# Performance work log

Hardware: AMD Instinct MI355X
Metric: run time of the kernel (lower is better)

## Reference

```python
import jax, jax.numpy as jnp
import numpy as np

CH = 128          # channels
R1 = 8            # ch_reduction1 -> theta/phi dim = 16
R2 = 2            # ch_reduction2 -> g dim = 64
D = 2             # downsampling (maxpool kernel/stride on w,h)


def _conv1x1x1(x, w, b):
    # x: (b, cin, n, w, h); w: (cout, cin); b: (cout,)
    return jnp.einsum('bcnwh,oc->bonwh', x, w) + b[None, :, None, None, None]


def _maxpool_wh(x):
    # 2x2 max pool (stride 2) over the last two dims; x: (b, c, n, w, h)
    b, c, n, w, h = x.shape
    return x.reshape(b, c, n, w // D, D, h // D, D).max(axis=(4, 6))


def setup_inputs() -> dict:
    key = jax.random.key(0)
    ks = jax.random.split(key, 9)
    c1, c2 = CH // R1, CH // R2
    s = lambda fan: 1.0 / np.sqrt(fan)
    return {
        'x': jax.random.normal(ks[0], (2, CH, 16, 32, 32), jnp.float32),
        'w_theta': jax.random.normal(ks[1], (c1, CH), jnp.float32) * s(CH),
        'b_theta': jnp.zeros((c1,), jnp.float32),
        'w_phi': jax.random.normal(ks[2], (c1, CH), jnp.float32) * s(CH),
        'b_phi': jnp.zeros((c1,), jnp.float32),
        'w_g': jax.random.normal(ks[3], (c2, CH), jnp.float32) * s(CH),
        'b_g': jnp.zeros((c2,), jnp.float32),
        'w_attn_g': jax.random.normal(ks[4], (CH, c2), jnp.float32) * s(c2),
        'b_attn_g': jnp.zeros((CH,), jnp.float32),
        'gamma': jnp.zeros((1,), jnp.float32),  # initial_gamma = 0
    }


def reference(x, w_theta, b_theta, w_phi, b_phi, w_g, b_g, w_attn_g, b_attn_g, gamma):
    bs, ch, n, w, h = x.shape
    N = n * w * h                       # query locations
    M = n * (w // D) * (h // D)         # pooled key/value locations

    # theta: (bs, N, c1)
    theta = jnp.tanh(_conv1x1x1(x, w_theta, b_theta))
    theta = theta.transpose(0, 2, 3, 4, 1).reshape(bs, N, -1)

    # phi: tanh proj -> maxpool over w,h -> (bs, M, c1)
    phi = _maxpool_wh(jnp.tanh(_conv1x1x1(x, w_phi, b_phi)))
    phi = phi.transpose(0, 2, 3, 4, 1).reshape(bs, M, -1)

    # dot-product kernel; softmax over dim=1 (QUERY axis), as in the torch code
    attn = jax.nn.softmax(jnp.einsum('bnc,bmc->bnm', theta, phi), axis=1)

    # g: proj -> maxpool -> (bs, M, c2)
    g = _maxpool_wh(_conv1x1x1(x, w_g, b_g))
    g = g.transpose(0, 2, 3, 4, 1).reshape(bs, M, -1)

    # attend and fold back to (bs, c2, n, w, h)
    attn_g = jnp.einsum('bnm,bmc->bnc', attn, g)
    attn_g = attn_g.reshape(bs, n, w, h, -1).transpose(0, 4, 1, 2, 3)
    attn_g = _conv1x1x1(attn_g, w_attn_g, b_attn_g)

    alpha = jax.nn.sigmoid(gamma)[0]
    out = (1.0 - alpha) * x + alpha * attn_g
    return (out, attn_g)
```

## Files before the change

### kernel.cpp

```cpp
#include <hip/hip_runtime.h>

typedef short bf16x8 __attribute__((ext_vector_type(8)));
typedef float f32x16 __attribute__((ext_vector_type(16)));

#define DI __device__ __forceinline__

constexpr int BS = 2, CH = 128;
constexpr int NQ = 16384, NM = 4096;
constexpr size_t NX = (size_t)BS * CH * NQ;

DI float bf2f(ushort u) { unsigned v = ((unsigned)u) << 16; return __builtin_bit_cast(float, v); }
DI ushort f2bf(float f) {
  unsigned u = __builtin_bit_cast(unsigned, f);
  u += 0x7FFFu + ((u >> 16) & 1u);
  return (ushort)(u >> 16);
}
DI float ldany(const void* p, size_t i, int f) {
  return f ? ((const float*)p)[i] : bf2f(((const ushort*)p)[i]);
}
DI f32x16 mfma_bf16(bf16x8 a, bf16x8 b, f32x16 c) {
  return __builtin_amdgcn_mfma_f32_32x32x16_bf16(a, b, c, 0, 0, 0);
}
DI float fexp2(float x) { return __builtin_amdgcn_exp2f(x); }

DI int sniff_local(const void* x) {
  const ushort* u = (const ushort*)x;
  int garbage = 0, zeros = 0;
  for (int i = 0; i < 256; ++i) {
    float v = bf2f(u[i]);
    if (!(fabsf(v) < 1e9f)) garbage++;
    if ((i & 1) == 0 && u[i] == 0) zeros++;
  }
  return (garbage >= 8 || zeros >= 100) ? 1 : 0;
}

__global__ __launch_bounds__(256) void k_prep(
    const void* __restrict__ x,
    const void* __restrict__ wT, const void* __restrict__ bT,
    const void* __restrict__ wP, const void* __restrict__ bP,
    const void* __restrict__ wG, const void* __restrict__ bG,
    const void* __restrict__ wAG, const void* __restrict__ bAG,
    int* __restrict__ flag,
    float* __restrict__ bAllf, uint4* __restrict__ wF, uint4* __restrict__ wBf)
{
  int t = threadIdx.x;
  __shared__ int fsh;
  if (t == 0) {
    int f = sniff_local(x);
    fsh = f;
    if (blockIdx.x == 0) flag[0] = f;
  }
  __syncthreads();
  int f = fsh;

  if (blockIdx.x == 0) {
    if (t < 16)  bAllf[t]       = ldany(bT, t, f);
    if (t < 16)  bAllf[16 + t]  = ldany(bP, t, f);
    if (t < 64)  bAllf[32 + t]  = ldany(bG, t, f);
    if (t < 128) bAllf[96 + t]  = ldany(bAG, t, f);
  } else if (blockIdx.x <= 4) {
    int idx = (blockIdx.x - 1) * 256 + t;
    int lane = idx & 63, ks = (idx >> 6) & 3, ot = idx >> 8;
    size_t src = (size_t)(ot * 32 + (lane & 31)) * 64 + ks * 16 + (lane >> 5) * 8;
    union { uint4 v4; ushort s[8]; } o;
    #pragma unroll
    for (int j = 0; j < 8; ++j) o.s[j] = f2bf(ldany(wAG, src + j, f));
    wF[idx] = o.v4;
  } else {
    int idx = (int)(blockIdx.x - 5) * 256 + t;
    int kb = idx / 192, rem = idx % 192;
    int ob = rem >> 6, lane = rem & 63;
    int r = ob * 32 + (lane & 31);
    int c = kb * 16 + (lane >> 5) * 8;
    const void* src; int row;
    if (r < 16)      { src = wT; row = r; }
    else if (r < 32) { src = wP; row = r - 16; }
    else             { src = wG; row = r - 32; }
    union { uint4 v4; ushort s[8]; } o;
    #pragma unroll
    for (int j = 0; j < 8; ++j) o.s[j] = f2bf(ldany(src, (size_t)row * 128 + c + j, f));
    wBf[(kb * 3 + ob) * 64 + lane] = o.v4;
  }
}

__global__ __launch_bounds__(256) void k_proj(
    const void* __restrict__ x, const int* __restrict__ flag,
    const uint4* __restrict__ wBf, const float* __restrict__ bAllf,
    ushort* __restrict__ theta, ushort* __restrict__ phi, ushort* __restrict__ gm)
{
  int b = blockIdx.y;
  int qt = blockIdx.x;
  int t = threadIdx.x;
  int w = t >> 6, l = t & 63, lr = l & 31, lh = l >> 5;
  int qhalf = w & 1, khalf = w >> 1;
  int f = flag[0];

  __shared__ float tile[64][33];

  size_t xbase = (size_t)b * CH * NQ + qt * 64 + qhalf * 32 + lr;

  f32x16 acc0, acc1, acc2;
  #pragma unroll
  for (int i = 0; i < 16; ++i) { acc0[i] = 0.f; acc1[i] = 0.f; acc2[i] = 0.f; }

  #pragma unroll
  for (int kk = 0; kk < 4; ++kk) {
    int kb = khalf * 4 + kk;
    union { uint4 v4; ushort s[8]; } a;
    int cb = kb * 16 + lh * 8;
    if (f) {
      const float* xf = (const float*)x;
      #pragma unroll
      for (int j = 0; j < 8; ++j) a.s[j] = f2bf(xf[xbase + (size_t)(cb + j) * NQ]);
    } else {
      const ushort* xu = (const ushort*)x;
      #pragma unroll
      for (int j = 0; j < 8; ++j) a.s[j] = xu[xbase + (size_t)(cb + j) * NQ];
    }
    bf16x8 aF = __builtin_bit_cast(bf16x8, a.v4);
    uint4 b0 = wBf[(kb * 3 + 0) * 64 + l];
    uint4 b1 = wBf[(kb * 3 + 1) * 64 + l];
    uint4 b2 = wBf[(kb * 3 + 2) * 64 + l];
    acc0 = mfma_bf16(aF, __builtin_bit_cast(bf16x8, b0), acc0);
    acc1 = mfma_bf16(aF, __builtin_bit_cast(bf16x8, b1), acc1);
    acc2 = mfma_bf16(aF, __builtin_bit_cast(bf16x8, b2), acc2);
  }

  constexpr float L2E = 1.4426950408889634f;

  #pragma unroll
  for (int ob = 0; ob < 3; ++ob) {
    f32x16 A = (ob == 0) ? acc0 : ((ob == 1) ? acc1 : acc2);
    __syncthreads();
    if (khalf == 1) {
      #pragma unroll
      for (int r = 0; r < 16; ++r) {
        int qq = (r & 3) + 8 * (r >> 2) + 4 * lh;
        tile[qhalf * 32 + qq][lr] = A[r];
      }
    }
    __syncthreads();
    if (khalf == 0) {
      #pragma unroll
      for (int r = 0; r < 16; ++r) {
        int qq = (r & 3) + 8 * (r >> 2) + 4 * lh;
        tile[qhalf * 32 + qq][lr] += A[r];
      }
    }
    __syncthreads();
    if (ob == 0) {
      if (t < 64) {
        union { uint4 v4[2]; ushort s[16]; } th;
        #pragma unroll
        for (int c = 0; c < 16; ++c)
          th.s[c] = f2bf(tanhf(tile[t][c] + bAllf[c]) * L2E);
        uint4* dst = (uint4*)(theta + ((size_t)b * NQ + qt * 64 + t) * 16);
        dst[0] = th.v4[0]; dst[1] = th.v4[1];
      } else if (t < 128) {
        int idx = t - 64;
        int m = idx >> 2, c4 = (idx & 3) * 4;
        int h2 = m * 2;
        union { uint2 v2; ushort s[4]; } ph;
        #pragma unroll
        for (int cc = 0; cc < 4; ++cc) {
          int c = 16 + c4 + cc;
          float z = fmaxf(fmaxf(tile[h2][c], tile[h2 + 1][c]),
                          fmaxf(tile[32 + h2][c], tile[32 + h2 + 1][c]));
          ph.s[cc] = f2bf(tanhf(z + bAllf[c]));
        }
        *(uint2*)(phi + ((size_t)b * NM + qt * 16 + m) * 16 + c4) = ph.v2;
      }
    } else {
      if (t < 128) {
        int cb = (ob - 1) * 32;
        int m = t >> 3, c4 = (t & 7) * 4;
        int h2 = m * 2;
        union { uint2 v2; ushort s[4]; } gv;
        #pragma unroll
        for (int cc = 0; cc < 4; ++cc) {
          int c = c4 + cc;
          float z = fmaxf(fmaxf(tile[h2][c], tile[h2 + 1][c]),
                          fmaxf(tile[32 + h2][c], tile[32 + h2 + 1][c]));
          gv.s[cc] = f2bf(z + bAllf[32 + cb + c]);
        }
        *(uint2*)(gm + ((size_t)b * NM + qt * 16 + m) * 64 + cb + c4) = gv.v2;
      }
    }
  }
}

__global__ __launch_bounds__(1024, 2) void k_denom2(
    const ushort* __restrict__ theta, const ushort* __restrict__ phi,
    const ushort* __restrict__ gm, uint4* __restrict__ gsF)
{
  int b = blockIdx.y, mb = blockIdx.x;
  int t = threadIdx.x;
  int w = t >> 6, l = t & 63, lr = l & 31, lh = l >> 5;
  int mbase = mb * 32;

  __shared__ float part[16][33];
  __shared__ float dinv_sh[32];
  __shared__ float tile[32][65];

  bf16x8 pB = __builtin_bit_cast(bf16x8, *(const uint4*)(phi + ((size_t)b * NM + mbase + lr) * 16 + lh * 8));
  const ushort* thb = theta + ((size_t)b * NQ + w * 1024 + lr) * 16 + lh * 8;

  bf16x8 tA1 = __builtin_bit_cast(bf16x8, *(const uint4*)(thb + 512));
  f32x16 S;
  #pragma unroll
  for (int i = 0; i < 16; ++i) S[i] = 0.f;
  S = mfma_bf16(__builtin_bit_cast(bf16x8, *(const uint4*)thb), pB, S);

  float s = 0.f;
  for (int it = 0; it < 32; ++it) {
    bf16x8 tA2 = __builtin_bit_cast(bf16x8, *(const uint4*)(thb + (size_t)((it + 2) & 31) * 512));
    __builtin_amdgcn_sched_barrier(0);
    f32x16 Sn;
    #pragma unroll
    for (int i = 0; i < 16; ++i) Sn[i] = 0.f;
    Sn = mfma_bf16(tA1, pB, Sn);
    #pragma unroll
    for (int r = 0; r < 16; ++r) s += fexp2(S[r]);
    S = Sn; tA1 = tA2;
  }
  s += __shfl_xor(s, 32, 64);
  if (l < 32) part[w][lr] = s;
  __syncthreads();

  if (t < 32) {
    float d = 0.f;
    #pragma unroll
    for (int p = 0; p < 16; ++p) d += part[p][t];
    dinv_sh[t] = 1.f / d;
  }
  __syncthreads();

  if (t < 256) {
    int m_loc = t >> 3, c = (t & 7) * 8;
    union { uint4 v4; ushort s[8]; } v;
    v.v4 = *(const uint4*)(gm + ((size_t)b * NM + mbase + m_loc) * 64 + c);
    float dv = dinv_sh[m_loc];
    #pragma unroll
    for (int j = 0; j < 8; ++j) tile[m_loc][c + j] = bf2f(v.s[j]) * dv;
  }
  __syncthreads();

  if (t < 256) {
    int ms_loc = t >> 7, ct = (t >> 6) & 1, lane = t & 63;
    int col = ct * 32 + (lane & 31);
    int rbase = ms_loc * 16 + (lane >> 5) * 8;
    union { uint4 v4; ushort s[8]; } o;
    #pragma unroll
    for (int j = 0; j < 8; ++j) o.s[j] = f2bf(tile[rbase + j][col]);
    int ms = (mbase >> 4) + ms_loc;
    gsF[(((size_t)b * 256 + ms) * 2 + ct) * 64 + lane] = o.v4;
  }
}

__global__ __launch_bounds__(256, 3) void k_attn(
    const ushort* __restrict__ theta, const ushort* __restrict__ phi,
    const uint4* __restrict__ gsF, const uint4* __restrict__ wF,
    const float* __restrict__ bAllf, const void* __restrict__ x,
    const void* __restrict__ gamma, const int* __restrict__ flag,
    void* __restrict__ out_base)
{
  int b = blockIdx.y;
  int q0 = blockIdx.x * 64;
  int t = threadIdx.x;
  int mq = t >> 6, l = t & 63, lr = l & 31, lh = l >> 5;

  __shared__ float agPart[4][32][65];
  __shared__ __align__(16) ushort agF[32][80];

  bf16x8 tB0 = __builtin_bit_cast(bf16x8, *(const uint4*)(theta + ((size_t)b * NQ + q0 + lr) * 16 + lh * 8));
  bf16x8 tB1 = __builtin_bit_cast(bf16x8, *(const uint4*)(theta + ((size_t)b * NQ + q0 + 32 + lr) * 16 + lh * 8));

  const ushort* phb = phi + ((size_t)b * NM + lr) * 16 + lh * 8;
  const uint4* gF = gsF + (size_t)b * 32768;

  f32x16 a00, a01, a10, a11;
  #pragma unroll
  for (int i = 0; i < 16; ++i) { a00[i] = 0.f; a01[i] = 0.f; a10[i] = 0.f; a11[i] = 0.f; }
  f32x16 zero16;
  #pragma unroll
  for (int i = 0; i < 16; ++i) zero16[i] = 0.f;

  size_t gb0 = (size_t)(mq * 2) * 128;
  uint4 g00 = gF[gb0 + l];
  uint4 g01 = gF[gb0 + 64 + l];
  uint4 g10 = gF[gb0 + 128 + l];
  uint4 g11 = gF[gb0 + 192 + l];
  bf16x8 pA = __builtin_bit_cast(bf16x8, *(const uint4*)(phb + (size_t)(mq * 32) * 16));

  for (int it = 0; it < 32; ++it) {
    int it1 = (it + 1) & 31;
    size_t gb = (size_t)(mq * 2 + it1 * 8) * 128;
    uint4 n00 = gF[gb + l];
    uint4 n01 = gF[gb + 64 + l];
    uint4 n10 = gF[gb + 128 + l];
    uint4 n11 = gF[gb + 192 + l];
    bf16x8 pAn = __builtin_bit_cast(bf16x8, *(const uint4*)(phb + (size_t)(mq * 32 + it1 * 128) * 16));
    __builtin_amdgcn_sched_barrier(0);

    f32x16 Sa = mfma_bf16(pA, tB0, zero16);
    f32x16 Sb = mfma_bf16(pA, tB1, zero16);

    uint u0, u1, u2, u3, u4, u5, u6, u7;

    #pragma unroll
    for (int r = 0; r < 16; ++r) Sa[r] = fexp2(Sa[r]);
    asm("v_cvt_pk_bf16_f32 %0, %1, %2" : "=v"(u0) : "v"(Sa[0]),  "v"(Sa[1]));
    asm("v_cvt_pk_bf16_f32 %0, %1, %2" : "=v"(u1) : "v"(Sa[2]),  "v"(Sa[3]));
    asm("v_cvt_pk_bf16_f32 %0, %1, %2" : "=v"(u2) : "v"(Sa[4]),  "v"(Sa[5]));
    asm("v_cvt_pk_bf16_f32 %0, %1, %2" : "=v"(u3) : "v"(Sa[6]),  "v"(Sa[7]));
    asm("v_cvt_pk_bf16_f32 %0, %1, %2" : "=v"(u4) : "v"(Sa[8]),  "v"(Sa[9]));
    asm("v_cvt_pk_bf16_f32 %0, %1, %2" : "=v"(u5) : "v"(Sa[10]), "v"(Sa[11]));
    asm("v_cvt_pk_bf16_f32 %0, %1, %2" : "=v"(u6) : "v"(Sa[12]), "v"(Sa[13]));
    asm("v_cvt_pk_bf16_f32 %0, %1, %2" : "=v"(u7) : "v"(Sa[14]), "v"(Sa[15]));
    asm("v_permlane32_swap_b32 %0, %1" : "+v"(u0), "+v"(u2));
    asm("v_permlane32_swap_b32 %0, %1" : "+v"(u1), "+v"(u3));
    asm("v_permlane32_swap_b32 %0, %1" : "+v"(u4), "+v"(u6));
    asm("v_permlane32_swap_b32 %0, %1" : "+v"(u5), "+v"(u7));
    {
      uint4 fa0 = make_uint4(u0, u1, u2, u3);
      uint4 fa1 = make_uint4(u4, u5, u6, u7);
      a00 = mfma_bf16(__builtin_bit_cast(bf16x8, fa0), __builtin_bit_cast(bf16x8, g00), a00);
      a01 = mfma_bf16(__builtin_bit_cast(bf16x8, fa0), __builtin_bit_cast(bf16x8, g01), a01);
      a00 = mfma_bf16(__builtin_bit_cast(bf16x8, fa1), __builtin_bit_cast(bf16x8, g10), a00);
      a01 = mfma_bf16(__builtin_bit_cast(bf16x8, fa1), __builtin_bit_cast(bf16x8, g11), a01);
    }

    #pragma unroll
    for (int r = 0; r < 16; ++r) Sb[r] = fexp2(Sb[r]);
    asm("v_cvt_pk_bf16_f32 %0, %1, %2" : "=v"(u0) : "v"(Sb[0]),  "v"(Sb[1]));
    asm("v_cvt_pk_bf16_f32 %0, %1, %2" : "=v"(u1) : "v"(Sb[2]),  "v"(Sb[3]));
    asm("v_cvt_pk_bf16_f32 %0, %1, %2" : "=v"(u2) : "v"(Sb[4]),  "v"(Sb[5]));
    asm("v_cvt_pk_bf16_f32 %0, %1, %2" : "=v"(u3) : "v"(Sb[6]),  "v"(Sb[7]));
    asm("v_cvt_pk_bf16_f32 %0, %1, %2" : "=v"(u4) : "v"(Sb[8]),  "v"(Sb[9]));
    asm("v_cvt_pk_bf16_f32 %0, %1, %2" : "=v"(u5) : "v"(Sb[10]), "v"(Sb[11]));
    asm("v_cvt_pk_bf16_f32 %0, %1, %2" : "=v"(u6) : "v"(Sb[12]), "v"(Sb[13]));
    asm("v_cvt_pk_bf16_f32 %0, %1, %2" : "=v"(u7) : "v"(Sb[14]), "v"(Sb[15]));
    asm("v_permlane32_swap_b32 %0, %1" : "+v"(u0), "+v"(u2));
    asm("v_permlane32_swap_b32 %0, %1" : "+v"(u1), "+v"(u3));
    asm("v_permlane32_swap_b32 %0, %1" : "+v"(u4), "+v"(u6));
    asm("v_permlane32_swap_b32 %0, %1" : "+v"(u5), "+v"(u7));
    {
      uint4 fb0 = make_uint4(u0, u1, u2, u3);
      uint4 fb1 = make_uint4(u4, u5, u6, u7);
      a10 = mfma_bf16(__builtin_bit_cast(bf16x8, fb0), __builtin_bit_cast(bf16x8, g00), a10);
      a11 = mfma_bf16(__builtin_bit_cast(bf16x8, fb0), __builtin_bit_cast(bf16x8, g01), a11);
      a10 = mfma_bf16(__builtin_bit_cast(bf16x8, fb1), __builtin_bit_cast(bf16x8, g10), a10);
      a11 = mfma_bf16(__builtin_bit_cast(bf16x8, fb1), __builtin_bit_cast(bf16x8, g11), a11);
    }

    pA = pAn;
    g00 = n00; g01 = n01; g10 = n10; g11 = n11;
  }

  int mode = flag[0];
  float ga = ldany(gamma, 0, mode);
  float alpha = 1.f / (1.f + __expf(-ga));

  #pragma unroll
  for (int h = 0; h < 2; ++h) {
    __syncthreads();
    {
      f32x16 ac0 = (h == 0) ? a00 : a10;
      f32x16 ac1 = (h == 0) ? a01 : a11;
      #pragma unroll
      for (int r = 0; r < 16; ++r) {
        int qq = (r & 3) + 8 * (r >> 2) + 4 * lh;
        agPart[mq][qq][lr]      = ac0[r];
        agPart[mq][qq][32 + lr] = ac1[r];
      }
    }
    __syncthreads();
    {
      #pragma unroll
      for (int jj = 0; jj < 8; ++jj) {
        int c = mq * 16 + lh * 8 + jj;
        float vsum = agPart[0][lr][c] + agPart[1][lr][c] + agPart[2][lr][c] + agPart[3][lr][c];
        agF[lr][c] = f2bf(vsum);
      }
    }
    __syncthreads();
    {
      f32x16 oacc;
      #pragma unroll
      for (int i = 0; i < 16; ++i) oacc[i] = 0.f;
      #pragma unroll
      for (int ks = 0; ks < 4; ++ks) {
        bf16x8 aw = __builtin_bit_cast(bf16x8, wF[(mq * 4 + ks) * 64 + l]);
        bf16x8 bg = __builtin_bit_cast(bf16x8, *(const uint4*)&agF[lr][ks * 16 + lh * 8]);
        oacc = mfma_bf16(aw, bg, oacc);
      }
      if (mode) {
        float* o0 = (float*)out_base;
        float* o1 = o0 + NX;
        const float* xf = (const float*)x;
        #pragma unroll
        for (int r = 0; r < 16; ++r) {
          int o = mq * 32 + (r & 3) + 8 * (r >> 2) + 4 * lh;
          size_t oi = ((size_t)b * CH + o) * NQ + q0 + h * 32 + lr;
          float ag = oacc[r] + bAllf[96 + o];
          o0[oi] = (1.f - alpha) * xf[oi] + alpha * ag;
          o1[oi] = ag;
        }
      } else {
        ushort* o0 = (ushort*)out_base;
        ushort* o1 = o0 + NX;
        const ushort* xu = (const ushort*)x;
        #pragma unroll
        for (int r = 0; r < 16; ++r) {
          int o = mq * 32 + (r & 3) + 8 * (r >> 2) + 4 * lh;
          size_t oi = ((size_t)b * CH + o) * NQ + q0 + h * 32 + lr;
          float ag = oacc[r] + bAllf[96 + o];
          o0[oi] = f2bf((1.f - alpha) * bf2f(xu[oi]) + alpha * ag);
          o1[oi] = f2bf(ag);
        }
      }
    }
  }
}

extern "C" void kernel_launch(void* const* d_in, const int* in_sizes, int n_in,
                              void* d_out, int out_size, void* d_ws, size_t ws_size,
                              hipStream_t stream) {
  const void* x    = d_in[0];
  const void* wT   = d_in[1];
  const void* bT   = d_in[2];
  const void* wP   = d_in[3];
  const void* bP   = d_in[4];
  const void* wG   = d_in[5];
  const void* bG   = d_in[6];
  const void* wAG  = d_in[7];
  const void* bAG  = d_in[8];
  const void* gmm  = d_in[9];

  char* ws = (char*)d_ws;
  ushort* theta  = (ushort*)(ws + 0);
  ushort* phi    = (ushort*)(ws + 1048576);
  ushort* gm     = (ushort*)(ws + 1310720);
  uint4*  gsF    = (uint4*) (ws + 3407872);
  uint4*  wF     = (uint4*) (ws + 4456448);
  uint4*  wBf    = (uint4*) (ws + 4472832);
  float*  bAllf  = (float*) (ws + 4497408);
  int*    flag   = (int*)   (ws + 4498432);

  k_prep<<<dim3(11), dim3(256), 0, stream>>>(x, wT, bT, wP, bP, wG, bG, wAG, bAG, flag, bAllf, wF, wBf);
  k_proj<<<dim3(256, 2), dim3(256), 0, stream>>>(x, flag, wBf, bAllf, theta, phi, gm);
  k_denom2<<<dim3(128, 2), dim3(1024), 0, stream>>>(theta, phi, gm, gsF);
  k_attn<<<dim3(256, 2), dim3(256), 0, stream>>>(theta, phi, gsF, wF, bAllf, x, gmm, flag, d_out);
}
```

Baseline: 73.21 us.

## Fold prep kernel into projection and attention kernels; remap attn blocks per XCD

Removes the separate k_prep launch. Each block of k_proj and k_attn now sniffs the input dtype in parallel and converts the weights and biases it needs into LDS. This eliminates one kernel launch and its serial dependency, and moves weight reads from global to LDS. In exchange every block repeats the weight conversion work. k_attn also switches to a 1D grid whose block index maps onto XCDs, so that each XCD handles contiguous query tiles of one batch for better L2 locality.

```diff
diff --git a/kernel.cpp b/kernel.cpp
--- a/kernel.cpp
+++ b/kernel.cpp
@@ -23,51 +23,40 @@
 }
 DI float fexp2(float x) { return __builtin_amdgcn_exp2f(x); }
 
-DI int sniff_local(const void* x) {
+DI int sniff_block(const void* x, int t, int* cnt_sh) {
   const ushort* u = (const ushort*)x;
-  int garbage = 0, zeros = 0;
-  for (int i = 0; i < 256; ++i) {
-    float v = bf2f(u[i]);
-    if (!(fabsf(v) < 1e9f)) garbage++;
-    if ((i & 1) == 0 && u[i] == 0) zeros++;
-  }
-  return (garbage >= 8 || zeros >= 100) ? 1 : 0;
-}
-
-__global__ __launch_bounds__(256) void k_prep(
+  if (t == 0) { cnt_sh[0] = 0; cnt_sh[1] = 0; }
+  __syncthreads();
+  if (t < 256) {
+    float v = bf2f(u[t]);
+    if (!(fabsf(v) < 1e9f)) atomicAdd(&cnt_sh[0], 1);
+    if (((t & 1) == 0) && (u[t] == 0)) atomicAdd(&cnt_sh[1], 1);
+  }
+  __syncthreads();
+  return (cnt_sh[0] >= 8 || cnt_sh[1] >= 100) ? 1 : 0;
+}
+
+__global__ __launch_bounds__(256) void k_proj(
     const void* __restrict__ x,
     const void* __restrict__ wT, const void* __restrict__ bT,
     const void* __restrict__ wP, const void* __restrict__ bP,
     const void* __restrict__ wG, const void* __restrict__ bG,
-    const void* __restrict__ wAG, const void* __restrict__ bAG,
-    int* __restrict__ flag,
-    float* __restrict__ bAllf, uint4* __restrict__ wF, uint4* __restrict__ wBf)
+    ushort* __restrict__ theta, ushort* __restrict__ phi, ushort* __restrict__ gm)
 {
+  int b = blockIdx.y;
+  int qt = blockIdx.x;
   int t = threadIdx.x;
-  __shared__ int fsh;
-  if (t == 0) {
-    int f = sniff_local(x);
-    fsh = f;
-    if (blockIdx.x == 0) flag[0] = f;
-  }
-  __syncthreads();
-  int f = fsh;
-
-  if (blockIdx.x == 0) {
-    if (t < 16)  bAllf[t]       = ldany(bT, t, f);
-    if (t < 16)  bAllf[16 + t]  = ldany(bP, t, f);
-    if (t < 64)  bAllf[32 + t]  = ldany(bG, t, f);
-    if (t < 128) bAllf[96 + t]  = ldany(bAG, t, f);
-  } else if (blockIdx.x <= 4) {
-    int idx = (blockIdx.x - 1) * 256 + t;
-    int lane = idx & 63, ks = (idx >> 6) & 3, ot = idx >> 8;
-    size_t src = (size_t)(ot * 32 + (lane & 31)) * 64 + ks * 16 + (lane >> 5) * 8;
-    union { uint4 v4; ushort s[8]; } o;
-    #pragma unroll
-    for (int j = 0; j < 8; ++j) o.s[j] = f2bf(ldany(wAG, src + j, f));
-    wF[idx] = o.v4;
-  } else {
-    int idx = (int)(blockIdx.x - 5) * 256 + t;
+  int w = t >> 6, l = t & 63, lr = l & 31, lh = l >> 5;
+  int qhalf = w & 1, khalf = w >> 1;
+
+  __shared__ int cnt_sh[2];
+  __shared__ __align__(16) uint4 wBf_sh[24][64];
+  __shared__ float bias_sh[96];
+  __shared__ float tile[64][33];
+
+  int f = sniff_block(x, t, cnt_sh);
+
+  for (int idx = t; idx < 1536; idx += 256) {
     int kb = idx / 192, rem = idx % 192;
     int ob = rem >> 6, lane = rem & 63;
     int r = ob * 32 + (lane & 31);
@@ -79,23 +68,12 @@
     union { uint4 v4; ushort s[8]; } o;
     #pragma unroll
     for (int j = 0; j < 8; ++j) o.s[j] = f2bf(ldany(src, (size_t)row * 128 + c + j, f));
-    wBf[(kb * 3 + ob) * 64 + lane] = o.v4;
-  }
-}
-
-__global__ __launch_bounds__(256) void k_proj(
-    const void* __restrict__ x, const int* __restrict__ flag,
-    const uint4* __restrict__ wBf, const float* __restrict__ bAllf,
-    ushort* __restrict__ theta, ushort* __restrict__ phi, ushort* __restrict__ gm)
-{
-  int b = blockIdx.y;
-  int qt = blockIdx.x;
-  int t = threadIdx.x;
-  int w = t >> 6, l = t & 63, lr = l & 31, lh = l >> 5;
-  int qhalf = w & 1, khalf = w >> 1;
-  int f = flag[0];
-
-  __shared__ float tile[64][33];
+    wBf_sh[kb * 3 + ob][lane] = o.v4;
+  }
+  if (t < 16)       bias_sh[t] = ldany(bT, t, f);
+  else if (t < 32)  bias_sh[t] = ldany(bP, t - 16, f);
+  else if (t < 96)  bias_sh[t] = ldany(bG, t - 32, f);
+  __syncthreads();
 
   size_t xbase = (size_t)b * CH * NQ + qt * 64 + qhalf * 32 + lr;
 
@@ -118,9 +96,9 @@
       for (int j = 0; j < 8; ++j) a.s[j] = xu[xbase + (size_t)(cb + j) * NQ];
     }
     bf16x8 aF = __builtin_bit_cast(bf16x8, a.v4);
-    uint4 b0 = wBf[(kb * 3 + 0) * 64 + l];
-    uint4 b1 = wBf[(kb * 3 + 1) * 64 + l];
-    uint4 b2 = wBf[(kb * 3 + 2) * 64 + l];
+    uint4 b0 = wBf_sh[kb * 3 + 0][l];
+    uint4 b1 = wBf_sh[kb * 3 + 1][l];
+    uint4 b2 = wBf_sh[kb * 3 + 2][l];
     acc0 = mfma_bf16(aF, __builtin_bit_cast(bf16x8, b0), acc0);
     acc1 = mfma_bf16(aF, __builtin_bit_cast(bf16x8, b1), acc1);
     acc2 = mfma_bf16(aF, __builtin_bit_cast(bf16x8, b2), acc2);
@@ -153,7 +131,7 @@
         union { uint4 v4[2]; ushort s[16]; } th;
         #pragma unroll
         for (int c = 0; c < 16; ++c)
-          th.s[c] = f2bf(tanhf(tile[t][c] + bAllf[c]) * L2E);
+          th.s[c] = f2bf(tanhf(tile[t][c] + bias_sh[c]) * L2E);
         uint4* dst = (uint4*)(theta + ((size_t)b * NQ + qt * 64 + t) * 16);
         dst[0] = th.v4[0]; dst[1] = th.v4[1];
       } else if (t < 128) {
@@ -166,7 +144,7 @@
           int c = 16 + c4 + cc;
           float z = fmaxf(fmaxf(tile[h2][c], tile[h2 + 1][c]),
                           fmaxf(tile[32 + h2][c], tile[32 + h2 + 1][c]));
-          ph.s[cc] = f2bf(tanhf(z + bAllf[c]));
+          ph.s[cc] = f2bf(tanhf(z + bias_sh[c]));
         }
         *(uint2*)(phi + ((size_t)b * NM + qt * 16 + m) * 16 + c4) = ph.v2;
       }
@@ -181,7 +159,7 @@
           int c = c4 + cc;
           float z = fmaxf(fmaxf(tile[h2][c], tile[h2 + 1][c]),
                           fmaxf(tile[32 + h2][c], tile[32 + h2 + 1][c]));
-          gv.s[cc] = f2bf(z + bAllf[32 + cb + c]);
+          gv.s[cc] = f2bf(z + bias_sh[32 + cb + c]);
         }
         *(uint2*)(gm + ((size_t)b * NM + qt * 16 + m) * 64 + cb + c4) = gv.v2;
       }
@@ -259,18 +237,35 @@
 
 __global__ __launch_bounds__(256, 3) void k_attn(
     const ushort* __restrict__ theta, const ushort* __restrict__ phi,
-    const uint4* __restrict__ gsF, const uint4* __restrict__ wF,
-    const float* __restrict__ bAllf, const void* __restrict__ x,
-    const void* __restrict__ gamma, const int* __restrict__ flag,
-    void* __restrict__ out_base)
+    const uint4* __restrict__ gsF, const void* __restrict__ wAG,
+    const void* __restrict__ bAG, const void* __restrict__ x,
+    const void* __restrict__ gamma, void* __restrict__ out_base)
 {
-  int b = blockIdx.y;
-  int q0 = blockIdx.x * 64;
+  int idx = blockIdx.x;
+  int xcd = idx & 7, slot = idx >> 3;
+  int b = xcd >> 2;
+  int q0 = ((xcd & 3) * 64 + slot) * 64;
   int t = threadIdx.x;
   int mq = t >> 6, l = t & 63, lr = l & 31, lh = l >> 5;
 
+  __shared__ int cnt_sh[2];
+  __shared__ __align__(16) uint4 wF_lds[16][64];
+  __shared__ float bag_sh[128];
   __shared__ float agPart[4][32][65];
   __shared__ __align__(16) ushort agF[32][80];
+
+  int f = sniff_block(x, t, cnt_sh);
+
+  for (int i = t; i < 1024; i += 256) {
+    int lane = i & 63, ks = (i >> 6) & 3, ot = i >> 8;
+    size_t src = (size_t)(ot * 32 + (lane & 31)) * 64 + ks * 16 + (lane >> 5) * 8;
+    union { uint4 v4; ushort s[8]; } o;
+    #pragma unroll
+    for (int j = 0; j < 8; ++j) o.s[j] = f2bf(ldany(wAG, src + j, f));
+    wF_lds[ot * 4 + ks][lane] = o.v4;
+  }
+  if (t < 128) bag_sh[t] = ldany(bAG, t, f);
+  __syncthreads();
 
   bf16x8 tB0 = __builtin_bit_cast(bf16x8, *(const uint4*)(theta + ((size_t)b * NQ + q0 + lr) * 16 + lh * 8));
   bf16x8 tB1 = __builtin_bit_cast(bf16x8, *(const uint4*)(theta + ((size_t)b * NQ + q0 + 32 + lr) * 16 + lh * 8));
@@ -357,8 +352,7 @@
     g00 = n00; g01 = n01; g10 = n10; g11 = n11;
   }
 
-  int mode = flag[0];
-  float ga = ldany(gamma, 0, mode);
+  float ga = ldany(gamma, 0, f);
   float alpha = 1.f / (1.f + __expf(-ga));
 
   #pragma unroll
@@ -390,11 +384,11 @@
       for (int i = 0; i < 16; ++i) oacc[i] = 0.f;
       #pragma unroll
       for (int ks = 0; ks < 4; ++ks) {
-        bf16x8 aw = __builtin_bit_cast(bf16x8, wF[(mq * 4 + ks) * 64 + l]);
+        bf16x8 aw = __builtin_bit_cast(bf16x8, wF_lds[mq * 4 + ks][l]);
         bf16x8 bg = __builtin_bit_cast(bf16x8, *(const uint4*)&agF[lr][ks * 16 + lh * 8]);
         oacc = mfma_bf16(aw, bg, oacc);
       }
-      if (mode) {
+      if (f) {
         float* o0 = (float*)out_base;
         float* o1 = o0 + NX;
         const float* xf = (const float*)x;
@@ -402,7 +396,7 @@
         for (int r = 0; r < 16; ++r) {
           int o = mq * 32 + (r & 3) + 8 * (r >> 2) + 4 * lh;
           size_t oi = ((size_t)b * CH + o) * NQ + q0 + h * 32 + lr;
-          float ag = oacc[r] + bAllf[96 + o];
+          float ag = oacc[r] + bag_sh[o];
           o0[oi] = (1.f - alpha) * xf[oi] + alpha * ag;
           o1[oi] = ag;
         }
@@ -414,7 +408,7 @@
         for (int r = 0; r < 16; ++r) {
           int o = mq * 32 + (r & 3) + 8 * (r >> 2) + 4 * lh;
           size_t oi = ((size_t)b * CH + o) * NQ + q0 + h * 32 + lr;
-          float ag = oacc[r] + bAllf[96 + o];
+          float ag = oacc[r] + bag_sh[o];
           o0[oi] = f2bf((1.f - alpha) * bf2f(xu[oi]) + alpha * ag);
           o1[oi] = f2bf(ag);
         }
@@ -442,13 +436,8 @@
   ushort* phi    = (ushort*)(ws + 1048576);
   ushort* gm     = (ushort*)(ws + 1310720);
   uint4*  gsF    = (uint4*) (ws + 3407872);
-  uint4*  wF     = (uint4*) (ws + 4456448);
-  uint4*  wBf    = (uint4*) (ws + 4472832);
-  float*  bAllf  = (float*) (ws + 4497408);
-  int*    flag   = (int*)   (ws + 4498432);
-
-  k_prep<<<dim3(11), dim3(256), 0, stream>>>(x, wT, bT, wP, bP, wG, bG, wAG, bAG, flag, bAllf, wF, wBf);
-  k_proj<<<dim3(256, 2), dim3(256), 0, stream>>>(x, flag, wBf, bAllf, theta, phi, gm);
+
+  k_proj<<<dim3(256, 2), dim3(256), 0, stream>>>(x, wT, bT, wP, bP, wG, bG, theta, phi, gm);
   k_denom2<<<dim3(128, 2), dim3(1024), 0, stream>>>(theta, phi, gm, gsF);
-  k_attn<<<dim3(256, 2), dim3(256), 0, stream>>>(theta, phi, gsF, wF, bAllf, x, gmm, flag, d_out);
-}
+  k_attn<<<dim3(512), dim3(256), 0, stream>>>(theta, phi, gsF, wAG, bAG, x, gmm, d_out);
+}
```

New measurement: 79.54 us. 1.09x slower.
